# Performance work log

Hardware: AMD Instinct MI355X
Metric: run time of the kernel (lower is better)

Reference implementation:

```python
import jax, jax.numpy as jnp
import numpy as np

B, S, H, R, VD, NC = 64, 512, 768, 256, 256, 9


def setup_inputs() -> dict:
    key = jax.random.key(0)
    ks = jax.random.split(key, 12)
    sequence_output = jax.random.normal(ks[0], (B, S, H), dtype=jnp.float32)
    visual_region_feats = jax.random.normal(ks[1], (B, R, VD), dtype=jnp.float32)
    # token bboxes: integer coords in [0, 1000], with x1<=x2, y1<=y2
    raw = jax.random.randint(ks[2], (B, S, 2, 2), 0, 1000)
    mn = raw.min(axis=2)  # [B,S,2] -> (xmin, ymin)
    mx = raw.max(axis=2)  # (xmax, ymax)
    bbox = jnp.stack([mn[..., 0], mn[..., 1], mx[..., 0], mx[..., 1]], axis=-1).astype(jnp.int64)
    # roi boxes: x1 in [0,700], width/height in [100,300]
    xy1 = jax.random.uniform(ks[3], (B, R, 2), minval=0.0, maxval=700.0)
    wh = jax.random.uniform(ks[4], (B, R, 2), minval=100.0, maxval=300.0)
    roi_boxes = jnp.concatenate([xy1, xy1 + wh], axis=-1).astype(jnp.float32)
    attention_mask = jnp.ones((B, S), dtype=jnp.int64)
    sc = 0.02
    W_proj = jax.random.normal(ks[5], (VD, H), dtype=jnp.float32) * sc
    b_proj = jnp.zeros((H,), dtype=jnp.float32)
    W_fuse = jax.random.normal(ks[6], (2 * H, H), dtype=jnp.float32) * sc
    b_fuse = jnp.zeros((H,), dtype=jnp.float32)
    W_h1 = jax.random.normal(ks[7], (H, 512), dtype=jnp.float32) * sc
    b_h1 = jnp.zeros((512,), dtype=jnp.float32)
    W_h2 = jax.random.normal(ks[8], (512, NC), dtype=jnp.float32) * sc
    b_h2 = jnp.zeros((NC,), dtype=jnp.float32)
    return dict(sequence_output=sequence_output, visual_region_feats=visual_region_feats,
                roi_boxes=roi_boxes, bbox=bbox, attention_mask=attention_mask,
                W_proj=W_proj, b_proj=b_proj, W_fuse=W_fuse, b_fuse=b_fuse,
                W_h1=W_h1, b_h1=b_h1, W_h2=W_h2, b_h2=b_h2)


def reference(sequence_output, visual_region_feats, roi_boxes, bbox, attention_mask,
              W_proj, b_proj, W_fuse, b_fuse, W_h1, b_h1, W_h2, b_h2):
    # visual projection: [B,R,VD] -> [B,R,H]
    vis = visual_region_feats @ W_proj + b_proj
    # containment mask [B,R,S]: token box fully inside roi box
    tb = bbox.astype(sequence_output.dtype)  # [B,S,4]
    rb = roi_boxes  # [B,R,4]
    inside = ((tb[:, None, :, 0] >= rb[:, :, None, 0]) &
              (tb[:, None, :, 2] <= rb[:, :, None, 2]) &
              (tb[:, None, :, 1] >= rb[:, :, None, 1]) &
              (tb[:, None, :, 3] <= rb[:, :, None, 3]))
    seq_len = sequence_output.shape[1]
    valid = (attention_mask == 1) & (jnp.arange(seq_len) >= 1)  # skip position 0 ([CLS])
    mask = (inside & valid[:, None, :]).astype(sequence_output.dtype)  # [B,R,S]
    cnt = mask.sum(axis=-1, keepdims=True)  # [B,R,1]
    # masked mean pool (empty regions -> zeros since numerator is 0)
    text = jnp.einsum('brs,bsh->brh', mask, sequence_output) / jnp.maximum(cnt, 1.0)
    fused = jax.nn.relu(jnp.concatenate([text, vis], axis=-1) @ W_fuse + b_fuse)
    h = jax.nn.relu(fused @ W_h1 + b_h1)
    logits = h @ W_h2 + b_h2  # [B,R,NC]
    return logits
```

## Files before the change

### kernel.cpp

```cpp
#include <hip/hip_runtime.h>
#include <hip/hip_bf16.h>


#define Bb 64
#define Ss 512
#define Hh 768
#define Rr 256
#define VDd 256
#define NCc 9

typedef __attribute__((ext_vector_type(8))) short short8v;
typedef __attribute__((ext_vector_type(4))) float f32x4;

__device__ __forceinline__ unsigned short f2bf(float v) {
    __hip_bfloat16 b = __float2bfloat16(v);
    return __builtin_bit_cast(unsigned short, b);
}
__device__ __forceinline__ float bf2f(unsigned short u) {
    return __bfloat162float(__builtin_bit_cast(__hip_bfloat16, u));
}

__device__ __forceinline__ void gll16(const void* g, void* l) {
    __builtin_amdgcn_global_load_lds(
        (const __attribute__((address_space(1))) void*)g,
        (__attribute__((address_space(3))) void*)l, 16, 0, 0);
}

__global__ __launch_bounds__(768) void weq_beq_kernel(
    const float* __restrict__ Wp, const float* __restrict__ bp,
    const float* __restrict__ Wf, const float* __restrict__ bf,
    float* __restrict__ Weq, float* __restrict__ beq)
{
    int n = threadIdx.x;
    int m = blockIdx.x;
    const float* Wfv = Wf + 768 * 768 + n;
    float acc = 0.f;
    if (m < 256) {
        const float* a = Wp + m * 768;
        #pragma unroll 4
        for (int k = 0; k < 768; ++k) acc += a[k] * Wfv[(size_t)k * 768];
        Weq[m * 768 + n] = acc;
    } else {
        #pragma unroll 4
        for (int k = 0; k < 768; ++k) acc += bp[k] * Wfv[(size_t)k * 768];
        beq[n] = bf[n] + acc;
    }
}

__global__ __launch_bounds__(256) void pool_kernel(
    const float* __restrict__ seq,
    const float* __restrict__ roi,
    const int*   __restrict__ bbox,
    const int*   __restrict__ amask,
    unsigned short* __restrict__ ah,
    unsigned short* __restrict__ al)
{
    int br = blockIdx.x;
    int b  = br >> 8;
    int tid = threadIdx.x;
    int wave = tid >> 6, lane = tid & 63;

    float4 rb = reinterpret_cast<const float4*>(roi)[br];

    __shared__ unsigned long long wm[8];
    __shared__ int s_idx[Ss];

    const int4* bb4 = reinterpret_cast<const int4*>(bbox) + (size_t)b * Ss;
    const int*  am  = amask + (size_t)b * Ss;

    for (int it = 0; it < 2; ++it) {
        int s = it * 256 + tid;
        bool pred = false;
        if (s >= 1 && am[s] == 1) {
            int4 tb = bb4[s];
            pred = ((float)tb.x >= rb.x) && ((float)tb.z <= rb.z) &&
                   ((float)tb.y >= rb.y) && ((float)tb.w <= rb.w);
        }
        unsigned long long mk = __ballot(pred);
        if (lane == 0) wm[it * 4 + wave] = mk;
    }
    __syncthreads();

    int pre[8]; int tot = 0;
    #pragma unroll
    for (int c = 0; c < 8; ++c) { pre[c] = tot; tot += __popcll(wm[c]); }

    #pragma unroll
    for (int it = 0; it < 2; ++it) {
        int c = it * 4 + wave;
        unsigned long long mk = wm[c];
        if ((mk >> lane) & 1ull) {
            int pos = pre[c] + __popcll(mk & ((1ull << lane) - 1ull));
            s_idx[pos] = c * 64 + lane;
        }
    }
    __syncthreads();

    float a0 = 0.f, a1 = 0.f, a2 = 0.f;
    for (int i = 0; i < tot; ++i) {
        const float* row = seq + ((size_t)b * Ss + s_idx[i]) * Hh;
        a0 += row[tid];
        a1 += row[tid + 256];
        a2 += row[tid + 512];
    }
    float inv = 1.f / fmaxf((float)tot, 1.f);
    a0 *= inv; a1 *= inv; a2 *= inv;

    size_t o = (size_t)br * 1024;
    unsigned short h0 = f2bf(a0), h1 = f2bf(a1), h2 = f2bf(a2);
    ah[o + tid]       = h0;  al[o + tid]       = f2bf(a0 - bf2f(h0));
    ah[o + tid + 256] = h1;  al[o + tid + 256] = f2bf(a1 - bf2f(h1));
    ah[o + tid + 512] = h2;  al[o + tid + 512] = f2bf(a2 - bf2f(h2));
}

__global__ __launch_bounds__(256) void feats_conv(
    const float* __restrict__ f, unsigned short* __restrict__ ah,
    unsigned short* __restrict__ al)
{
    int m = blockIdx.x, c = threadIdx.x;
    float v = f[(size_t)m * VDd + c];
    size_t o = (size_t)m * 1024 + 768 + c;
    unsigned short h = f2bf(v);
    ah[o] = h;
    al[o] = f2bf(v - bf2f(h));
}

__global__ __launch_bounds__(256) void tconv_kernel(
    const float* __restrict__ src, int Ns,
    unsigned short* __restrict__ dh, unsigned short* __restrict__ dl,
    int ldd, int co)
{
    __shared__ float t[32][33];
    int k0 = blockIdx.x * 32, n0 = blockIdx.y * 32;
    int tx = threadIdx.x & 31, ty = threadIdx.x >> 5;
    #pragma unroll
    for (int i = 0; i < 4; ++i)
        t[ty + i * 8][tx] = src[(size_t)(k0 + ty + i * 8) * Ns + n0 + tx];
    __syncthreads();
    #pragma unroll
    for (int i = 0; i < 4; ++i) {
        int n = n0 + ty + i * 8;
        int k = k0 + tx;
        float v = t[tx][ty + i * 8];
        size_t o = (size_t)n * ldd + co + k;
        unsigned short h = f2bf(v);
        dh[o] = h;
        dl[o] = f2bf(v - bf2f(h));
    }
}

__global__ __launch_bounds__(256) void gemm_mfma(
    const unsigned short* __restrict__ Ah, const unsigned short* __restrict__ Al, int lda,
    const unsigned short* __restrict__ Bh, const unsigned short* __restrict__ Bl, int ldb,
    int K, const float* __restrict__ bias, int epi,
    unsigned short* __restrict__ Ch, unsigned short* __restrict__ Cl,
    float* __restrict__ Cf, int ldc)
{
    __shared__ __align__(16) unsigned char lds[32768];
    const int ATH = 0, ATL = 8192, BTH = 16384, BTL = 24576;

    const int tid  = threadIdx.x;
    const int w    = tid >> 6, lane = tid & 63;
    const int m0   = blockIdx.y * 128, n0 = blockIdx.x * 128;

    const int wm0 = (w >> 1) * 64, wn0 = (w & 1) * 64;
    const int fr  = lane & 15;
    const int kg  = lane >> 4;

    f32x4 acc[4][4] = {};

    const int srow_base = w * 32;
    const int rsub = lane >> 2;
    const int cd   = lane & 3;

    for (int k0 = 0; k0 < K; k0 += 32) {
        __syncthreads();
        #pragma unroll
        for (int i = 0; i < 2; ++i) {
            int row = srow_base + i * 16 + rsub;
            int cs  = cd ^ ((row >> 1) & 3);
            int lo  = (srow_base + i * 16) * 64 + lane * 16;
            size_t ga = (size_t)(m0 + row) * lda + k0 + cs * 8;
            size_t gb = (size_t)(n0 + row) * ldb + k0 + cs * 8;
            gll16(Ah + ga, lds + ATH + lo);
            gll16(Al + ga, lds + ATL + lo);
            gll16(Bh + gb, lds + BTH + lo);
            gll16(Bl + gb, lds + BTL + lo);
        }
        __syncthreads();

        short8v fah[4], fal[4], fbh[4], fbl[4];
        #pragma unroll
        for (int f = 0; f < 4; ++f) {
            int ar = wm0 + f * 16 + fr;
            int ao = ar * 64 + (kg ^ ((ar >> 1) & 3)) * 16;
            fah[f] = *(const short8v*)(lds + ATH + ao);
            fal[f] = *(const short8v*)(lds + ATL + ao);
            int br = wn0 + f * 16 + fr;
            int bo = br * 64 + (kg ^ ((br >> 1) & 3)) * 16;
            fbh[f] = *(const short8v*)(lds + BTH + bo);
            fbl[f] = *(const short8v*)(lds + BTL + bo);
        }
        #pragma unroll
        for (int fm = 0; fm < 4; ++fm)
            #pragma unroll
            for (int fn = 0; fn < 4; ++fn) {
                acc[fm][fn] = __builtin_amdgcn_mfma_f32_16x16x32_bf16(fah[fm], fbh[fn], acc[fm][fn], 0, 0, 0);
                acc[fm][fn] = __builtin_amdgcn_mfma_f32_16x16x32_bf16(fah[fm], fbl[fn], acc[fm][fn], 0, 0, 0);
                acc[fm][fn] = __builtin_amdgcn_mfma_f32_16x16x32_bf16(fal[fm], fbh[fn], acc[fm][fn], 0, 0, 0);
            }
    }

    #pragma unroll
    for (int fn = 0; fn < 4; ++fn) {
        int col = n0 + wn0 + fn * 16 + fr;
        float bv = bias[col];
        #pragma unroll
        for (int fm = 0; fm < 4; ++fm) {
            int rowb = m0 + wm0 + fm * 16 + kg * 4;
            #pragma unroll
            for (int j = 0; j < 4; ++j) {
                float v = fmaxf(acc[fm][fn][j] + bv, 0.f);
                size_t o = (size_t)(rowb + j) * ldc + col;
                if (epi) {
                    unsigned short h = f2bf(v);
                    Ch[o] = h;
                    Cl[o] = f2bf(v - bf2f(h));
                } else {
                    Cf[o] = v;
                }
            }
        }
    }
}

__global__ __launch_bounds__(256) void logits_kernel(
    const float* __restrict__ h, const float* __restrict__ W2,
    const float* __restrict__ b2, float* __restrict__ out)
{
    __shared__ float w2s[512 * NCc];
    for (int i = threadIdx.x; i < 512 * NCc; i += 256) w2s[i] = W2[i];
    __syncthreads();

    int wave = threadIdx.x >> 6, lane = threadIdx.x & 63;
    int row = blockIdx.x * 4 + wave;
    const float* hr = h + (size_t)row * 512;

    float p[NCc] = {};
    #pragma unroll
    for (int j = 0; j < 8; ++j) {
        int k = lane + 64 * j;
        float hv = hr[k];
        const float* wrow = &w2s[k * NCc];
        #pragma unroll
        for (int n = 0; n < NCc; ++n) p[n] += hv * wrow[n];
    }
    #pragma unroll
    for (int off = 32; off > 0; off >>= 1) {
        #pragma unroll
        for (int n = 0; n < NCc; ++n) p[n] += __shfl_down(p[n], off);
    }
    if (lane == 0) {
        float* orow = out + (size_t)row * NCc;
        #pragma unroll
        for (int n = 0; n < NCc; ++n) orow[n] = p[n] + b2[n];
    }
}

extern "C" void kernel_launch(void* const* d_in, const int* in_sizes, int n_in,
                              void* d_out, int out_size, void* d_ws, size_t ws_size,
                              hipStream_t stream)
{
    const float* seq   = (const float*)d_in[0];
    const float* feats = (const float*)d_in[1];
    const float* roi   = (const float*)d_in[2];
    const int*   bbox  = (const int*)d_in[3];
    const int*   amask = (const int*)d_in[4];
    const float* Wp = (const float*)d_in[5];
    const float* bp = (const float*)d_in[6];
    const float* Wf = (const float*)d_in[7];
    const float* bf = (const float*)d_in[8];
    const float* W1 = (const float*)d_in[9];
    const float* b1 = (const float*)d_in[10];
    const float* W2 = (const float*)d_in[11];
    const float* b2 = (const float*)d_in[12];
    float* out = (float*)d_out;

    char* ws = (char*)d_ws;
    unsigned short* A_hi  = (unsigned short*)(ws);
    unsigned short* A_lo  = (unsigned short*)(ws + 33554432);
    unsigned short* fu_hi = (unsigned short*)(ws + 67108864);
    unsigned short* fu_lo = (unsigned short*)(ws + 92274688);
    unsigned short* Bf_hi = (unsigned short*)(ws + 117440512);
    unsigned short* Bf_lo = (unsigned short*)(ws + 119013376);
    unsigned short* B1_hi = (unsigned short*)(ws + 120586240);
    unsigned short* B1_lo = (unsigned short*)(ws + 121372672);
    float*          Weq   = (float*)(ws + 122159104);
    float*          beq   = (float*)(ws + 122945536);
    float*          hbuf  = (float*)(ws);

    weq_beq_kernel<<<257, 768, 0, stream>>>(Wp, bp, Wf, bf, Weq, beq);
    pool_kernel<<<Bb * Rr, 256, 0, stream>>>(seq, roi, bbox, amask, A_hi, A_lo);
    feats_conv<<<Bb * Rr, VDd, 0, stream>>>(feats, A_hi, A_lo);
    tconv_kernel<<<dim3(24, 24), 256, 0, stream>>>(Wf, 768, Bf_hi, Bf_lo, 1024, 0);
    tconv_kernel<<<dim3(8, 24), 256, 0, stream>>>(Weq, 768, Bf_hi, Bf_lo, 1024, 768);
    tconv_kernel<<<dim3(24, 16), 256, 0, stream>>>(W1, 512, B1_hi, B1_lo, 768, 0);

    gemm_mfma<<<dim3(768 / 128, 16384 / 128), 256, 0, stream>>>(
        A_hi, A_lo, 1024, Bf_hi, Bf_lo, 1024, 1024, beq, 1,
        fu_hi, fu_lo, nullptr, 768);
    gemm_mfma<<<dim3(512 / 128, 16384 / 128), 256, 0, stream>>>(
        fu_hi, fu_lo, 768, B1_hi, B1_lo, 768, 768, b1, 0,
        nullptr, nullptr, hbuf, 512);

    logits_kernel<<<(Bb * Rr) / 4, 256, 0, stream>>>(hbuf, W2, b2, out);
}
```

Baseline: 484.0 us.

## Double-buffer LDS tiles in MFMA GEMM and swizzle workgroup order across XCDs

The split-bf16 MFMA GEMM now keeps two 32 KB LDS stages and issues the global-to-LDS loads for the next K-tile before computing on the current one, with one barrier per iteration instead of two. The aim is to hide global load latency behind the MFMA work. Workgroup IDs are also remapped so that consecutive tiles are grouped per XCD (8 chiplets), which should improve L2 reuse. The cost is doubled LDS use (64 KB per block), which lowers occupancy. The swizzle assumes the grid size is divisible by 8.

```diff
diff --git a/kernel.cpp b/kernel.cpp
--- a/kernel.cpp
+++ b/kernel.cpp
@@ -156,12 +156,18 @@
     unsigned short* __restrict__ Ch, unsigned short* __restrict__ Cl,
     float* __restrict__ Cf, int ldc)
 {
-    __shared__ __align__(16) unsigned char lds[32768];
+    __shared__ __align__(16) unsigned char lds[65536];
     const int ATH = 0, ATL = 8192, BTH = 16384, BTL = 24576;
 
     const int tid  = threadIdx.x;
     const int w    = tid >> 6, lane = tid & 63;
-    const int m0   = blockIdx.y * 128, n0 = blockIdx.x * 128;
+
+    const int nwg  = gridDim.x * gridDim.y;
+    const int cpx  = nwg >> 3;
+    const int orig = blockIdx.y * gridDim.x + blockIdx.x;
+    const int swz  = (orig & 7) * cpx + (orig >> 3);
+    const int m0   = (swz / gridDim.x) * 128;
+    const int n0   = (swz % gridDim.x) * 128;
 
     const int wm0 = (w >> 1) * 64, wn0 = (w & 1) * 64;
     const int fr  = lane & 15;
@@ -173,33 +179,40 @@
     const int rsub = lane >> 2;
     const int cd   = lane & 3;
 
-    for (int k0 = 0; k0 < K; k0 += 32) {
-        __syncthreads();
+    auto STAGE = [&](int bo, int kk) {
         #pragma unroll
         for (int i = 0; i < 2; ++i) {
             int row = srow_base + i * 16 + rsub;
             int cs  = cd ^ ((row >> 1) & 3);
             int lo  = (srow_base + i * 16) * 64 + lane * 16;
-            size_t ga = (size_t)(m0 + row) * lda + k0 + cs * 8;
-            size_t gb = (size_t)(n0 + row) * ldb + k0 + cs * 8;
-            gll16(Ah + ga, lds + ATH + lo);
-            gll16(Al + ga, lds + ATL + lo);
-            gll16(Bh + gb, lds + BTH + lo);
-            gll16(Bl + gb, lds + BTL + lo);
-        }
-        __syncthreads();
+            size_t ga = (size_t)(m0 + row) * lda + kk + cs * 8;
+            size_t gb = (size_t)(n0 + row) * ldb + kk + cs * 8;
+            gll16(Ah + ga, lds + bo + ATH + lo);
+            gll16(Al + ga, lds + bo + ATL + lo);
+            gll16(Bh + gb, lds + bo + BTH + lo);
+            gll16(Bl + gb, lds + bo + BTL + lo);
+        }
+    };
+
+    const int nt = K >> 5;
+    STAGE(0, 0);
+    __syncthreads();
+
+    for (int t = 0; t < nt; ++t) {
+        const int cur = (t & 1) << 15;
+        if (t + 1 < nt) STAGE(cur ^ 32768, (t + 1) << 5);
 
         short8v fah[4], fal[4], fbh[4], fbl[4];
         #pragma unroll
         for (int f = 0; f < 4; ++f) {
             int ar = wm0 + f * 16 + fr;
             int ao = ar * 64 + (kg ^ ((ar >> 1) & 3)) * 16;
-            fah[f] = *(const short8v*)(lds + ATH + ao);
-            fal[f] = *(const short8v*)(lds + ATL + ao);
+            fah[f] = *(const short8v*)(lds + cur + ATH + ao);
+            fal[f] = *(const short8v*)(lds + cur + ATL + ao);
             int br = wn0 + f * 16 + fr;
             int bo = br * 64 + (kg ^ ((br >> 1) & 3)) * 16;
-            fbh[f] = *(const short8v*)(lds + BTH + bo);
-            fbl[f] = *(const short8v*)(lds + BTL + bo);
+            fbh[f] = *(const short8v*)(lds + cur + BTH + bo);
+            fbl[f] = *(const short8v*)(lds + cur + BTL + bo);
         }
         #pragma unroll
         for (int fm = 0; fm < 4; ++fm)
@@ -209,6 +222,7 @@
                 acc[fm][fn] = __builtin_amdgcn_mfma_f32_16x16x32_bf16(fah[fm], fbl[fn], acc[fm][fn], 0, 0, 0);
                 acc[fm][fn] = __builtin_amdgcn_mfma_f32_16x16x32_bf16(fal[fm], fbh[fn], acc[fm][fn], 0, 0, 0);
             }
+        __syncthreads();
     }
 
     #pragma unroll
```

After: 459.7 us. 5.0% less time.

## Rewrite split-bf16 GEMMs as multi-stage pipelined 8-wave kernels and fuse feats conversion

Applied to the files above, without the earlier changes.

Replaces the 128x128, 256-thread split-bf16 GEMM with a templated 512-thread kernel using 256-wide N tiles. It uses a 4-buffer LDS ring with global_load_lds prefetch three stages ahead, vmcnt-based waits, a workgroup swizzle, and raised wave priority around the MFMA blocks. The three hi/lo product terms become three sequential K passes over different operand pairs instead of three MFMAs per step. Separately, the visual-feature bf16 split is folded into the pool kernel, removing one launch. This aims to hide memory latency and improve operand reuse, at the cost of more LDS per block, higher register pressure (FM=8 gives 32 accumulators per wave), and lower occupancy.

```diff
diff --git a/kernel.cpp b/kernel.cpp
--- a/kernel.cpp
+++ b/kernel.cpp
@@ -12,15 +12,14 @@
 typedef __attribute__((ext_vector_type(8))) short short8v;
 typedef __attribute__((ext_vector_type(4))) float f32x4;
 
-__device__ __forceinline__ unsigned short f2bf(float v) {
+static __device__ __forceinline__ unsigned short f2bf(float v) {
     __hip_bfloat16 b = __float2bfloat16(v);
     return __builtin_bit_cast(unsigned short, b);
 }
-__device__ __forceinline__ float bf2f(unsigned short u) {
+static __device__ __forceinline__ float bf2f(unsigned short u) {
     return __bfloat162float(__builtin_bit_cast(__hip_bfloat16, u));
 }
-
-__device__ __forceinline__ void gll16(const void* g, void* l) {
+static __device__ __forceinline__ void gll16(const void* g, void* l) {
     __builtin_amdgcn_global_load_lds(
         (const __attribute__((address_space(1))) void*)g,
         (__attribute__((address_space(3))) void*)l, 16, 0, 0);
@@ -52,6 +51,7 @@
     const float* __restrict__ roi,
     const int*   __restrict__ bbox,
     const int*   __restrict__ amask,
+    const float* __restrict__ feats,
     unsigned short* __restrict__ ah,
     unsigned short* __restrict__ al)
 {
@@ -111,18 +111,10 @@
     ah[o + tid]       = h0;  al[o + tid]       = f2bf(a0 - bf2f(h0));
     ah[o + tid + 256] = h1;  al[o + tid + 256] = f2bf(a1 - bf2f(h1));
     ah[o + tid + 512] = h2;  al[o + tid + 512] = f2bf(a2 - bf2f(h2));
-}
-
-__global__ __launch_bounds__(256) void feats_conv(
-    const float* __restrict__ f, unsigned short* __restrict__ ah,
-    unsigned short* __restrict__ al)
-{
-    int m = blockIdx.x, c = threadIdx.x;
-    float v = f[(size_t)m * VDd + c];
-    size_t o = (size_t)m * 1024 + 768 + c;
-    unsigned short h = f2bf(v);
-    ah[o] = h;
-    al[o] = f2bf(v - bf2f(h));
+    float fv = feats[(size_t)br * VDd + tid];
+    unsigned short fh = f2bf(fv);
+    ah[o + 768 + tid] = fh;
+    al[o + 768 + tid] = f2bf(fv - bf2f(fh));
 }
 
 __global__ __launch_bounds__(256) void tconv_kernel(
@@ -149,75 +141,115 @@
     }
 }
 
-__global__ __launch_bounds__(256) void gemm_mfma(
+template<int FM>
+__global__ __launch_bounds__(512) void gemm8p(
     const unsigned short* __restrict__ Ah, const unsigned short* __restrict__ Al, int lda,
     const unsigned short* __restrict__ Bh, const unsigned short* __restrict__ Bl, int ldb,
     int K, const float* __restrict__ bias, int epi,
     unsigned short* __restrict__ Ch, unsigned short* __restrict__ Cl,
     float* __restrict__ Cf, int ldc)
 {
-    __shared__ __align__(16) unsigned char lds[32768];
-    const int ATH = 0, ATL = 8192, BTH = 16384, BTL = 24576;
+    constexpr int BM  = FM * 32;
+    constexpr int ACH = BM / 16;
+    constexpr int AIN = ACH / 8;
+    constexpr int ASZ = BM * 64;
+    constexpr int BUF = ASZ + 16384;
+    __shared__ __align__(16) unsigned char lds[4 * BUF];
 
     const int tid  = threadIdx.x;
     const int w    = tid >> 6, lane = tid & 63;
-    const int m0   = blockIdx.y * 128, n0 = blockIdx.x * 128;
-
-    const int wm0 = (w >> 1) * 64, wn0 = (w & 1) * 64;
-    const int fr  = lane & 15;
-    const int kg  = lane >> 4;
-
-    f32x4 acc[4][4] = {};
-
-    const int srow_base = w * 32;
-    const int rsub = lane >> 2;
-    const int cd   = lane & 3;
-
-    for (int k0 = 0; k0 < K; k0 += 32) {
-        __syncthreads();
+    const int wm   = w >> 2, wn = w & 3;
+    const int fr   = lane & 15, kg = lane >> 4;
+    const int rsub = lane >> 2, cd = lane & 3;
+
+    const int gx   = gridDim.x;
+    const int nwg  = gx * gridDim.y;
+    const int cpx  = nwg >> 3;
+    const int orig = blockIdx.y * gx + blockIdx.x;
+    const int swz  = (orig & 7) * cpx + (orig >> 3);
+    const int m0   = (swz / gx) * BM;
+    const int n0   = (swz % gx) * 256;
+
+    const int TPS = K >> 5;
+    const int NT  = 3 * TPS;
+
+    int st_seg = 0, st_kp = 0, st_buf = 0;
+    auto STAGE = [&]() {
+        const unsigned short* As = (st_seg == 2) ? Al : Ah;
+        const unsigned short* Bs = (st_seg == 1) ? Bl : Bh;
+        unsigned char* base = lds + st_buf * BUF;
+        #pragma unroll
+        for (int i = 0; i < AIN; ++i) {
+            int cc = w * AIN + i;
+            int r  = cc * 16 + rsub;
+            int cs = cd ^ ((r >> 1) & 3);
+            gll16(As + (size_t)(m0 + r) * lda + st_kp + cs * 8,
+                  base + cc * 1024 + lane * 16);
+        }
         #pragma unroll
         for (int i = 0; i < 2; ++i) {
-            int row = srow_base + i * 16 + rsub;
-            int cs  = cd ^ ((row >> 1) & 3);
-            int lo  = (srow_base + i * 16) * 64 + lane * 16;
-            size_t ga = (size_t)(m0 + row) * lda + k0 + cs * 8;
-            size_t gb = (size_t)(n0 + row) * ldb + k0 + cs * 8;
-            gll16(Ah + ga, lds + ATH + lo);
-            gll16(Al + ga, lds + ATL + lo);
-            gll16(Bh + gb, lds + BTH + lo);
-            gll16(Bl + gb, lds + BTL + lo);
-        }
-        __syncthreads();
-
-        short8v fah[4], fal[4], fbh[4], fbl[4];
-        #pragma unroll
-        for (int f = 0; f < 4; ++f) {
-            int ar = wm0 + f * 16 + fr;
-            int ao = ar * 64 + (kg ^ ((ar >> 1) & 3)) * 16;
-            fah[f] = *(const short8v*)(lds + ATH + ao);
-            fal[f] = *(const short8v*)(lds + ATL + ao);
-            int br = wn0 + f * 16 + fr;
-            int bo = br * 64 + (kg ^ ((br >> 1) & 3)) * 16;
-            fbh[f] = *(const short8v*)(lds + BTH + bo);
-            fbl[f] = *(const short8v*)(lds + BTL + bo);
-        }
-        #pragma unroll
-        for (int fm = 0; fm < 4; ++fm)
+            int cc = w * 2 + i;
+            int r  = cc * 16 + rsub;
+            int cs = cd ^ ((r >> 1) & 3);
+            gll16(Bs + (size_t)(n0 + r) * ldb + st_kp + cs * 8,
+                  base + ASZ + cc * 1024 + lane * 16);
+        }
+        st_kp += 32;
+        if (st_kp >= K) { st_kp = 0; ++st_seg; }
+        st_buf = (st_buf + 1) & 3;
+    };
+
+    f32x4 acc[FM][4] = {};
+
+    STAGE(); STAGE(); STAGE();
+
+    for (int t = 0; t < NT; ++t) {
+        if (t < NT - 2) {
+            if constexpr (FM == 8)
+                asm volatile("s_waitcnt vmcnt(8)\n\ts_barrier" ::: "memory");
+            else
+                asm volatile("s_waitcnt vmcnt(6)\n\ts_barrier" ::: "memory");
+        } else {
+            asm volatile("s_waitcnt vmcnt(0)\n\ts_barrier" ::: "memory");
+        }
+        if (t + 3 < NT) STAGE();
+
+        const unsigned char* bufA = lds + (t & 3) * BUF;
+        const unsigned char* bufB = bufA + ASZ;
+
+        short8v bfrag[4];
+        #pragma unroll
+        for (int fn = 0; fn < 4; ++fn) {
+            int br = wn * 64 + fn * 16 + fr;
+            bfrag[fn] = *(const short8v*)(bufB + br * 64 + ((kg ^ ((br >> 1) & 3)) << 4));
+        }
+        #pragma unroll
+        for (int ph = 0; ph < FM / 4; ++ph) {
+            if (ph) asm volatile("s_barrier" ::: "memory");
+            short8v afrag[4];
             #pragma unroll
-            for (int fn = 0; fn < 4; ++fn) {
-                acc[fm][fn] = __builtin_amdgcn_mfma_f32_16x16x32_bf16(fah[fm], fbh[fn], acc[fm][fn], 0, 0, 0);
-                acc[fm][fn] = __builtin_amdgcn_mfma_f32_16x16x32_bf16(fah[fm], fbl[fn], acc[fm][fn], 0, 0, 0);
-                acc[fm][fn] = __builtin_amdgcn_mfma_f32_16x16x32_bf16(fal[fm], fbh[fn], acc[fm][fn], 0, 0, 0);
+            for (int q = 0; q < 4; ++q) {
+                int ar = wm * (FM * 16) + (ph * 4 + q) * 16 + fr;
+                afrag[q] = *(const short8v*)(bufA + ar * 64 + ((kg ^ ((ar >> 1) & 3)) << 4));
             }
+            __builtin_amdgcn_s_setprio(1);
+            #pragma unroll
+            for (int q = 0; q < 4; ++q)
+                #pragma unroll
+                for (int fn = 0; fn < 4; ++fn)
+                    acc[ph * 4 + q][fn] = __builtin_amdgcn_mfma_f32_16x16x32_bf16(
+                        afrag[q], bfrag[fn], acc[ph * 4 + q][fn], 0, 0, 0);
+            __builtin_amdgcn_s_setprio(0);
+        }
     }
 
     #pragma unroll
     for (int fn = 0; fn < 4; ++fn) {
-        int col = n0 + wn0 + fn * 16 + fr;
+        int col = n0 + wn * 64 + fn * 16 + fr;
         float bv = bias[col];
         #pragma unroll
-        for (int fm = 0; fm < 4; ++fm) {
-            int rowb = m0 + wm0 + fm * 16 + kg * 4;
+        for (int fm = 0; fm < FM; ++fm) {
+            int rowb = m0 + wm * (FM * 16) + fm * 16 + kg * 4;
             #pragma unroll
             for (int j = 0; j < 4; ++j) {
                 float v = fmaxf(acc[fm][fn][j] + bv, 0.f);
@@ -300,16 +332,15 @@
     float*          hbuf  = (float*)(ws);
 
     weq_beq_kernel<<<257, 768, 0, stream>>>(Wp, bp, Wf, bf, Weq, beq);
-    pool_kernel<<<Bb * Rr, 256, 0, stream>>>(seq, roi, bbox, amask, A_hi, A_lo);
-    feats_conv<<<Bb * Rr, VDd, 0, stream>>>(feats, A_hi, A_lo);
+    pool_kernel<<<Bb * Rr, 256, 0, stream>>>(seq, roi, bbox, amask, feats, A_hi, A_lo);
     tconv_kernel<<<dim3(24, 24), 256, 0, stream>>>(Wf, 768, Bf_hi, Bf_lo, 1024, 0);
     tconv_kernel<<<dim3(8, 24), 256, 0, stream>>>(Weq, 768, Bf_hi, Bf_lo, 1024, 768);
     tconv_kernel<<<dim3(24, 16), 256, 0, stream>>>(W1, 512, B1_hi, B1_lo, 768, 0);
 
-    gemm_mfma<<<dim3(768 / 128, 16384 / 128), 256, 0, stream>>>(
+    gemm8p<8><<<dim3(768 / 256, 16384 / 256), 512, 0, stream>>>(
         A_hi, A_lo, 1024, Bf_hi, Bf_lo, 1024, 1024, beq, 1,
         fu_hi, fu_lo, nullptr, 768);
-    gemm_mfma<<<dim3(512 / 128, 16384 / 128), 256, 0, stream>>>(
+    gemm8p<4><<<dim3(512 / 256, 16384 / 128), 512, 0, stream>>>(
         fu_hi, fu_lo, 768, B1_hi, B1_lo, 768, 768, b1, 0,
         nullptr, nullptr, hbuf, 512);
 
```

Measured after the change: 487.8 us. No clear change (+0.8%).
